# Kernel tuning notes

Measured on AMD Instinct MI355X. Metric: run time of the kernel, lower is better.

## Reference

```python
import jax, jax.numpy as jnp
import numpy as np

B, N, D = 8, 2048, 1024


def setup_inputs() -> dict:
    key = jax.random.key(0)
    k = jax.random.split(key, 6)
    scale = 1.0 / np.sqrt(D)
    x = jax.random.normal(k[0], (B, N, D), dtype=jnp.float32)
    attention_mask = jax.random.randint(k[1], (B, N, N), 0, 2, dtype=jnp.int32)
    W_qkv = jax.random.normal(k[2], (D, 3 * D), dtype=jnp.float32) * scale
    b_qkv = jax.random.normal(k[3], (3 * D,), dtype=jnp.float32) * 0.01
    W_out = jax.random.normal(k[4], (D, D), dtype=jnp.float32) * scale
    b_out = jax.random.normal(k[5], (D,), dtype=jnp.float32) * 0.01
    return {"x": x, "attention_mask": attention_mask, "W_qkv": W_qkv,
            "b_qkv": b_qkv, "W_out": W_out, "b_out": b_out}


def reference(x, attention_mask, W_qkv, b_qkv, W_out, b_out):
    # QKV projection: [B,N,3D]
    qkv = jnp.einsum('bnd,de->bne', x, W_qkv) + b_qkv
    Q, K, V = jnp.split(qkv, 3, axis=-1)
    inv_sqrt_d = jnp.float32(1.0 / np.sqrt(D))
    # naive full [B,N,N] attention scores
    scores = jnp.einsum('bqd,bkd->bqk', Q, K) * inv_sqrt_d
    w = jax.nn.softmax(scores, axis=-1)
    # masked_fill(mask == 0, -1e20) then renormalize (module applies softmax
    # again over the masked weights; dropout is identity in eval mode)
    w = jnp.where(attention_mask == 0, jnp.float32(-1e20), w)
    w = jax.nn.softmax(w, axis=-1)
    out = jnp.einsum('bqk,bkd->bqd', w, V)
    return jnp.einsum('bnd,de->bne', out, W_out) + b_out
```

## Files before the change

kernel.cpp:

```cpp
#include <hip/hip_runtime.h>
#include <hip/hip_bf16.h>

typedef __attribute__((ext_vector_type(8))) short short8;
typedef __attribute__((ext_vector_type(4))) float floatx4;
typedef __attribute__((ext_vector_type(8))) int intx8;

#define AS_GLOBAL(p) ((const __attribute__((address_space(1))) void*)(p))
#define AS_LOCAL(p)  ((__attribute__((address_space(3))) void*)(p))

__device__ __forceinline__ float b2f(unsigned short u) {
    union { unsigned int u; float f; } c; c.u = ((unsigned int)u) << 16; return c.f;
}
__device__ __forceinline__ unsigned short f2b(float f) {
    union { float f; unsigned int u; } c; c.f = f;
    unsigned int u = c.u;
    unsigned int r = (u + 0x7fffu + ((u >> 16) & 1u)) >> 16;
    return (unsigned short)r;
}
__device__ __forceinline__ unsigned char f2fp8(float v) {
    return (unsigned char)(__builtin_amdgcn_cvt_pk_fp8_f32(v, v, 0, false) & 0xff);
}

__global__ __launch_bounds__(256) void cast_x(
    const float* __restrict__ in, unsigned short* __restrict__ xbf,
    unsigned int* __restrict__ xf8, int n4) {
    int i = blockIdx.x * 256 + threadIdx.x;
    if (i >= n4) return;
    float4 v = ((const float4*)in)[i];
    ushort4 o;
    o.x = f2b(v.x); o.y = f2b(v.y); o.z = f2b(v.z); o.w = f2b(v.w);
    ((ushort4*)xbf)[i] = o;
    int p = __builtin_amdgcn_cvt_pk_fp8_f32(v.x, v.y, 0, false);
    p = __builtin_amdgcn_cvt_pk_fp8_f32(v.z, v.w, p, true);
    xf8[i] = (unsigned int)p;
}

__global__ __launch_bounds__(256) void transpose_f32_bf16(
    const float* __restrict__ in, unsigned short* __restrict__ out, int R, int C) {
    __shared__ float t[32][33];
    int c0 = blockIdx.x * 32, r0 = blockIdx.y * 32;
    int tx = threadIdx.x, ty = threadIdx.y;
#pragma unroll
    for (int k = 0; k < 32; k += 8)
        t[ty + k][tx] = in[(size_t)(r0 + ty + k) * C + c0 + tx];
    __syncthreads();
#pragma unroll
    for (int k = 0; k < 32; k += 8)
        out[(size_t)(c0 + ty + k) * R + r0 + tx] = f2b(t[tx][ty + k]);
}

__global__ __launch_bounds__(256) void transpose_f32_fp8_qk(
    const float* __restrict__ in, unsigned char* __restrict__ out) {
    __shared__ float t[32][33];
    int c0 = blockIdx.x * 32, r0 = blockIdx.y * 32;
    int tx = threadIdx.x, ty = threadIdx.y;
#pragma unroll
    for (int k = 0; k < 32; k += 8)
        t[ty + k][tx] = in[(size_t)(r0 + ty + k) * 3072 + c0 + tx];
    __syncthreads();
#pragma unroll
    for (int k = 0; k < 32; k += 8)
        out[(size_t)(c0 + ty + k) * 1024 + r0 + tx] = f2fp8(t[tx][ty + k]);
}

__global__ __launch_bounds__(256) void cast_wv(
    const float* __restrict__ in, unsigned short* __restrict__ out) {
    int i = blockIdx.x * 256 + threadIdx.x;
    int d = i >> 8, rem = (i & 255) * 4;
    float4 v = *(const float4*)&in[(size_t)d * 3072 + 2048 + rem];
    ushort4 o;
    o.x = f2b(v.x); o.y = f2b(v.y); o.z = f2b(v.z); o.w = f2b(v.w);
    *(ushort4*)&out[(size_t)d * 1024 + rem] = o;
}

__global__ __launch_bounds__(256) void bvo_kernel(
    const unsigned short* __restrict__ WoT, const float* __restrict__ bqkv,
    const float* __restrict__ bout, float* __restrict__ bvo) {
    int wv = threadIdx.x >> 6, lane = threadIdx.x & 63;
    int e = blockIdx.x * 4 + wv;
    const unsigned short* row = WoT + (size_t)e * 1024;
    float s = 0.f;
    for (int h = lane; h < 1024; h += 64) s += b2f(row[h]) * bqkv[2048 + h];
#pragma unroll
    for (int o = 32; o; o >>= 1) s += __shfl_xor(s, o);
    if (lane == 0) bvo[e] = s + bout[e];
}

__global__ __launch_bounds__(256) void softmax2_kernel(
    unsigned short* __restrict__ S, const int* __restrict__ mask) {
    const int N = 2048;
    int wv = threadIdx.x >> 6, lane = threadIdx.x & 63;
    size_t row = (size_t)blockIdx.x * 4 + wv;
    unsigned short* srow = S + row * N;
    const int* mrow = mask + row * N;

    float e1[32];
    float l = 0.f;
#pragma unroll
    for (int i = 0; i < 4; ++i) {
        uint4 raw = ((const uint4*)srow)[lane + 64 * i];
        unsigned v[4] = { raw.x, raw.y, raw.z, raw.w };
#pragma unroll
        for (int j = 0; j < 4; ++j) {
            float a = b2f((unsigned short)(v[j] & 0xffff));
            float bb = b2f((unsigned short)(v[j] >> 16));
            float ea = __expf(a), eb = __expf(bb);
            e1[i * 8 + 2 * j] = ea; e1[i * 8 + 2 * j + 1] = eb;
            l += ea + eb;
        }
    }
#pragma unroll
    for (int o = 32; o; o >>= 1) l += __shfl_xor(l, o);
    float invl = 1.0f / l;

    float e2[32];
    float z = 0.f;
#pragma unroll
    for (int i = 0; i < 4; ++i) {
        uint4 m0 = ((const uint4*)mrow)[2 * (lane + 64 * i)];
        uint4 m1 = ((const uint4*)mrow)[2 * (lane + 64 * i) + 1];
        int mk[8] = { (int)m0.x, (int)m0.y, (int)m0.z, (int)m0.w,
                      (int)m1.x, (int)m1.y, (int)m1.z, (int)m1.w };
#pragma unroll
        for (int j = 0; j < 8; ++j) {
            float w1 = e1[i * 8 + j] * invl;
            float e = mk[j] ? __expf(w1) : 0.0f;
            e2[i * 8 + j] = e; z += e;
        }
    }
#pragma unroll
    for (int o = 32; o; o >>= 1) z += __shfl_xor(z, o);
    float invz = (z > 0.f) ? 1.0f / z : 0.0f;
    float fallback = 1.0f / N;
#pragma unroll
    for (int i = 0; i < 4; ++i) {
        float p[8];
#pragma unroll
        for (int j = 0; j < 8; ++j)
            p[j] = (z > 0.f) ? e2[i * 8 + j] * invz : fallback;
        uint4 o;
        o.x = (unsigned)f2b(p[0]) | ((unsigned)f2b(p[1]) << 16);
        o.y = (unsigned)f2b(p[2]) | ((unsigned)f2b(p[3]) << 16);
        o.z = (unsigned)f2b(p[4]) | ((unsigned)f2b(p[5]) << 16);
        o.w = (unsigned)f2b(p[6]) | ((unsigned)f2b(p[7]) << 16);
        ((uint4*)srow)[lane + 64 * i] = o;
    }
}

template <int TAG, bool BIAS, int OUT, int XS, int YS>
__global__ __launch_bounds__(256) void gemm_bt(
    const unsigned short* __restrict__ A, int ldA, long long strideA,
    const unsigned short* __restrict__ B, int ldB, long long strideB,
    void* __restrict__ C, int ldC, long long strideC,
    const float* __restrict__ bias, float scale, int K) {
    __shared__ __align__(16) unsigned short lds[2 * 128 * 64];
    unsigned short* At = lds;
    unsigned short* Bt = lds + 128 * 64;

    unsigned flat = blockIdx.x;
    unsigned wg = (flat & 7u) * (gridDim.x >> 3) + (flat >> 3);
    int bx = wg & ((1u << XS) - 1u);
    int by = (wg >> XS) & ((1u << YS) - 1u);
    int bz = wg >> (XS + YS);

    const unsigned short* Ab = A + (size_t)bz * strideA;
    const unsigned short* Bb = B + (size_t)bz * strideB;
    int tn0 = bx * 128;
    int tm0 = by * 128;
    int tid = threadIdx.x;
    int wave = tid >> 6, lane = tid & 63;
    int lm = lane & 15, q = lane >> 4;
    int wm = (wave >> 1) * 64, wn = (wave & 1) * 64;

    int srow = lane >> 3;
    int sblk = lane & 7;

    floatx4 acc[4][4] = {};

    for (int k0 = 0; k0 < K; k0 += 64) {
        __syncthreads();
#pragma unroll
        for (int i = 0; i < 4; ++i) {
            int chunk = wave * 4 + i;
            int r = chunk * 8 + srow;
            int blk = sblk ^ (r & 7);
            const unsigned short* ga = Ab + (size_t)(tm0 + r) * ldA + (k0 + blk * 8);
            __builtin_amdgcn_global_load_lds(AS_GLOBAL(ga), AS_LOCAL(At + chunk * 512), 16, 0, 0);
            const unsigned short* gb = Bb + (size_t)(tn0 + r) * ldB + (k0 + blk * 8);
            __builtin_amdgcn_global_load_lds(AS_GLOBAL(gb), AS_LOCAL(Bt + chunk * 512), 16, 0, 0);
        }
        __syncthreads();
#pragma unroll
        for (int kk = 0; kk < 2; ++kk) {
            short8 af[4], bf[4];
#pragma unroll
            for (int mt = 0; mt < 4; ++mt) {
                int r = wm + mt * 16 + lm;
                af[mt] = *(const short8*)(At + r * 64 + (((kk * 4 + q) ^ (r & 7)) * 8));
            }
#pragma unroll
            for (int nt = 0; nt < 4; ++nt) {
                int r = wn + nt * 16 + lm;
                bf[nt] = *(const short8*)(Bt + r * 64 + (((kk * 4 + q) ^ (r & 7)) * 8));
            }
#pragma unroll
            for (int mt = 0; mt < 4; ++mt)
#pragma unroll
                for (int nt = 0; nt < 4; ++nt)
                    acc[mt][nt] = __builtin_amdgcn_mfma_f32_16x16x32_bf16(
                        af[mt], bf[nt], acc[mt][nt], 0, 0, 0);
        }
    }

    float biasv[4];
#pragma unroll
    for (int nt = 0; nt < 4; ++nt)
        biasv[nt] = BIAS ? bias[tn0 + wn + nt * 16 + lm] : 0.0f;

    if (OUT == 2) {
        __syncthreads();
        unsigned short* T = lds;
#pragma unroll
        for (int mt = 0; mt < 4; ++mt)
#pragma unroll
            for (int nt = 0; nt < 4; ++nt) {
                int n = wn + nt * 16 + lm;
                int m0 = wm + mt * 16 + q * 4;
                int col = m0 ^ ((n & 15) << 3);
                ushort4 pv;
                float v0 = acc[mt][nt][0] * scale; if (BIAS) v0 += biasv[nt];
                float v1 = acc[mt][nt][1] * scale; if (BIAS) v1 += biasv[nt];
                float v2 = acc[mt][nt][2] * scale; if (BIAS) v2 += biasv[nt];
                float v3 = acc[mt][nt][3] * scale; if (BIAS) v3 += biasv[nt];
                pv.x = f2b(v0); pv.y = f2b(v1); pv.z = f2b(v2); pv.w = f2b(v3);
                *(ushort4*)&T[n * 128 + col] = pv;
            }
        __syncthreads();
        unsigned short* Cb = (unsigned short*)C + (size_t)(tm0 >> 11) * strideC + (tm0 & 2047);
#pragma unroll
        for (int r8 = 0; r8 < 8; ++r8) {
            int idx = tid + 256 * r8;
            int d = idx >> 4, c = idx & 15;
            int cs = (c ^ (d & 15)) << 3;
            short8 v = *(const short8*)&T[d * 128 + cs];
            *(short8*)&Cb[(size_t)(tn0 + d) * ldC + c * 8] = v;
        }
        return;
    }

#pragma unroll
    for (int mt = 0; mt < 4; ++mt) {
#pragma unroll
        for (int nt = 0; nt < 4; ++nt) {
            int gm = tm0 + wm + mt * 16 + q * 4;
            int gn = tn0 + wn + nt * 16 + lm;
#pragma unroll
            for (int r = 0; r < 4; ++r) {
                float v = acc[mt][nt][r] * scale;
                if (BIAS) v += biasv[nt];
                size_t idx = (size_t)bz * strideC + (size_t)(gm + r) * ldC + gn;
                if (OUT == 1) ((float*)C)[idx] = v;
                else          ((unsigned short*)C)[idx] = f2b(v);
            }
        }
    }
}

template <int TAG, bool BIAS, bool OUTFP8, int XS, int YS>
__global__ __launch_bounds__(256) void gemm_f8_bt(
    const unsigned char* __restrict__ A, int ldA, long long strideA,
    const unsigned char* __restrict__ B, int ldB, long long strideB,
    void* __restrict__ C, int ldC, long long strideC,
    const float* __restrict__ bias, float scale, int K) {
    __shared__ __align__(16) unsigned char lds[2 * 128 * 128];
    unsigned char* At = lds;
    unsigned char* Bt = lds + 128 * 128;

    unsigned flat = blockIdx.x;
    unsigned wg = (flat & 7u) * (gridDim.x >> 3) + (flat >> 3);
    int bx = wg & ((1u << XS) - 1u);
    int by = (wg >> XS) & ((1u << YS) - 1u);
    int bz = wg >> (XS + YS);

    const unsigned char* Ab = A + (size_t)bz * strideA;
    const unsigned char* Bb = B + (size_t)bz * strideB;
    int tn0 = bx * 128;
    int tm0 = by * 128;
    int tid = threadIdx.x;
    int wave = tid >> 6, lane = tid & 63;
    int lm = lane & 15, q = lane >> 4;
    int q2 = q * 2;
    int wm = (wave >> 1) * 64, wn = (wave & 1) * 64;

    int srow = lane >> 3;
    int sblk = lane & 7;

    floatx4 acc[4][4] = {};

    for (int k0 = 0; k0 < K; k0 += 128) {
        __syncthreads();
#pragma unroll
        for (int i = 0; i < 4; ++i) {
            int chunk = wave * 4 + i;
            int r = chunk * 8 + srow;
            int blk = sblk ^ (r & 7);
            const unsigned char* ga = Ab + (size_t)(tm0 + r) * ldA + (k0 + blk * 16);
            __builtin_amdgcn_global_load_lds(AS_GLOBAL(ga), AS_LOCAL(At + chunk * 1024), 16, 0, 0);
            const unsigned char* gb = Bb + (size_t)(tn0 + r) * ldB + (k0 + blk * 16);
            __builtin_amdgcn_global_load_lds(AS_GLOBAL(gb), AS_LOCAL(Bt + chunk * 1024), 16, 0, 0);
        }
        __syncthreads();
        intx8 af[4], bf[4];
#pragma unroll
        for (int mt = 0; mt < 4; ++mt) {
            int r = wm + mt * 16 + lm;
            const unsigned char* base = At + r * 128;
            int4 lo = *(const int4*)(base + ((q2 ^ (r & 7)) << 4));
            int4 hi = *(const int4*)(base + (((q2 + 1) ^ (r & 7)) << 4));
            af[mt][0] = lo.x; af[mt][1] = lo.y; af[mt][2] = lo.z; af[mt][3] = lo.w;
            af[mt][4] = hi.x; af[mt][5] = hi.y; af[mt][6] = hi.z; af[mt][7] = hi.w;
        }
#pragma unroll
        for (int nt = 0; nt < 4; ++nt) {
            int r = wn + nt * 16 + lm;
            const unsigned char* base = Bt + r * 128;
            int4 lo = *(const int4*)(base + ((q2 ^ (r & 7)) << 4));
            int4 hi = *(const int4*)(base + (((q2 + 1) ^ (r & 7)) << 4));
            bf[nt][0] = lo.x; bf[nt][1] = lo.y; bf[nt][2] = lo.z; bf[nt][3] = lo.w;
            bf[nt][4] = hi.x; bf[nt][5] = hi.y; bf[nt][6] = hi.z; bf[nt][7] = hi.w;
        }
#pragma unroll
        for (int mt = 0; mt < 4; ++mt)
#pragma unroll
            for (int nt = 0; nt < 4; ++nt)
                acc[mt][nt] = __builtin_amdgcn_mfma_scale_f32_16x16x128_f8f6f4(
                    af[mt], bf[nt], acc[mt][nt], 0, 0,
                    0, 0x7f7f7f7f, 0, 0x7f7f7f7f);
    }

    float biasv[4];
#pragma unroll
    for (int nt = 0; nt < 4; ++nt)
        biasv[nt] = BIAS ? bias[tn0 + wn + nt * 16 + lm] : 0.0f;
#pragma unroll
    for (int mt = 0; mt < 4; ++mt) {
#pragma unroll
        for (int nt = 0; nt < 4; ++nt) {
            int gm = tm0 + wm + mt * 16 + q * 4;
            int gn = tn0 + wn + nt * 16 + lm;
#pragma unroll
            for (int r = 0; r < 4; ++r) {
                float v = acc[mt][nt][r] * scale;
                if (BIAS) v += biasv[nt];
                size_t idx = (size_t)bz * strideC + (size_t)(gm + r) * ldC + gn;
                if (OUTFP8) ((unsigned char*)C)[idx] = f2fp8(v);
                else        ((unsigned short*)C)[idx] = f2b(v);
            }
        }
    }
}

extern "C" void kernel_launch(void* const* d_in, const int* in_sizes, int n_in,
                              void* d_out, int out_size, void* d_ws, size_t ws_size,
                              hipStream_t stream) {
    const float* x    = (const float*)d_in[0];
    const int*   mask = (const int*)d_in[1];
    const float* Wqkv = (const float*)d_in[2];
    const float* bqkv = (const float*)d_in[3];
    const float* Wout = (const float*)d_in[4];
    const float* bout = (const float*)d_in[5];
    float* out = (float*)d_out;

    char* w = (char*)d_ws;
    unsigned short* x_bf  = (unsigned short*)(w);
    unsigned char*  x_f8  = (unsigned char*)(w + 33554432);
    unsigned char*  QKf8  = (unsigned char*)(w + 50331648);
    unsigned short* VpT   = (unsigned short*)(w + 117440512);
    unsigned short* S     = (unsigned short*)(w + 150994944);
    unsigned char*  WqkT8 = (unsigned char*)(w + 218103808);
    unsigned short* WoT   = (unsigned short*)(w + 220200960);
    unsigned short* Wv_bf = (unsigned short*)(w + 222298112);
    unsigned short* WvoT  = (unsigned short*)(w + 224395264);
    float*          bvo   = (float*)(w + 226492416);

    cast_x<<<16384, 256, 0, stream>>>(x, x_bf, (unsigned int*)x_f8, 4194304);
    transpose_f32_fp8_qk<<<dim3(64, 32), dim3(32, 8), 0, stream>>>(Wqkv, WqkT8);
    transpose_f32_bf16<<<dim3(32, 32), dim3(32, 8), 0, stream>>>(Wout, WoT, 1024, 1024);
    cast_wv<<<1024, 256, 0, stream>>>(Wqkv, Wv_bf);
    bvo_kernel<<<256, 256, 0, stream>>>(WoT, bqkv, bout, bvo);

    gemm_bt<4, false, 0, 3, 3><<<64, 256, 0, stream>>>(
        WoT, 1024, 0, Wv_bf, 1024, 0, WvoT, 1024, 0, nullptr, 1.0f, 1024);

    gemm_f8_bt<0, true, true, 4, 7><<<2048, 256, 0, stream>>>(
        x_f8, 1024, 0, WqkT8, 1024, 0, QKf8, 2048, 0, bqkv, 1.0f, 1024);

    gemm_bt<5, true, 2, 3, 7><<<1024, 256, 0, stream>>>(
        x_bf, 1024, 0, WvoT, 1024, 0, VpT, 2048, 1024LL * 2048, bvo, 1.0f, 1024);

    gemm_f8_bt<1, false, false, 4, 4><<<2048, 256, 0, stream>>>(
        QKf8, 2048, 2048LL * 2048, QKf8 + 1024, 2048, 2048LL * 2048,
        S, 2048, 2048LL * 2048, nullptr, 0.03125f, 1024);

    softmax2_kernel<<<4096, 256, 0, stream>>>(S, mask);

    gemm_bt<2, false, 1, 3, 4><<<1024, 256, 0, stream>>>(
        S, 2048, 2048LL * 2048, VpT, 2048, 1024LL * 2048,
        out, 1024, 2048LL * 1024, nullptr, 1.0f, 2048);
}
```

Before: 530.2 us.

## Add 256x256-tile 8-wave bf16 GEMM with double-buffered LDS for PV product

Replaces the final attention-times-V GEMM (previously 128x128 tiles, 256 threads) with a new kernel using 256x256 output tiles, 8 waves, and double-buffered LDS filled through direct global-to-LDS loads with an XOR swizzle. Loads for the next K-tile are interleaved with four MFMA phases separated by barriers and priority bumps. The goal is higher arithmetic intensity and better overlap of memory with MFMA. In exchange it uses 128KB of LDS and a large accumulator register footprint, and the grid shrinks to 256 blocks, which may underfill the CUs.

```diff
diff --git a/kernel.cpp b/kernel.cpp
--- a/kernel.cpp
+++ b/kernel.cpp
@@ -266,6 +266,160 @@
     }
 }
 
+template <int MH>
+__device__ __forceinline__ void mfma16(floatx4 (&acc)[8][4], const short8 (&af)[4],
+                                       const short8 (&bf)[4]) {
+#pragma unroll
+    for (int m = 0; m < 4; ++m)
+#pragma unroll
+        for (int n = 0; n < 4; ++n)
+            acc[MH * 4 + m][n] = __builtin_amdgcn_mfma_f32_16x16x32_bf16(
+                af[m], bf[n], acc[MH * 4 + m][n], 0, 0, 0);
+}
+
+template <int NXB, int NYB>
+__global__ __launch_bounds__(512, 2) void gemm_bt8(
+    const unsigned short* __restrict__ A, int ldA, long long strideA,
+    const unsigned short* __restrict__ B, int ldB, long long strideB,
+    float* __restrict__ C, int ldC, long long strideC,
+    float scale, int K) {
+    __shared__ __align__(16) unsigned short lds[65536];
+    constexpr int TILE = 16384;
+    constexpr int BREG = 32768;
+
+    int tid = threadIdx.x;
+    int wave = tid >> 6, lane = tid & 63;
+    int lm = lane & 15, q = lane >> 4;
+    int wmi = wave >> 2, wni = wave & 3;
+
+    unsigned flat = blockIdx.x;
+    unsigned wg = (flat & 7u) * (gridDim.x >> 3) + (flat >> 3);
+    int bx = wg % NXB;
+    int rem = wg / NXB;
+    int by = rem % NYB;
+    int bz = rem / NYB;
+    int tn0 = bx * 256, tm0 = by * 256;
+
+    const unsigned short* Ab = A + (size_t)bz * strideA;
+    const unsigned short* Bb = B + (size_t)bz * strideB;
+
+    int srow8 = lane >> 3, s7 = lane & 7;
+    const unsigned short* gA[4];
+    const unsigned short* gB[4];
+#pragma unroll
+    for (int i = 0; i < 4; ++i) {
+        int r = i * 64 + wave * 8 + srow8;
+        int blk = s7 ^ (r & 7);
+        gA[i] = Ab + (size_t)(tm0 + r) * ldA + blk * 8;
+        gB[i] = Bb + (size_t)(tn0 + r) * ldB + blk * 8;
+    }
+
+    int nt = K >> 6;
+
+#pragma unroll
+    for (int i = 0; i < 4; ++i)
+        __builtin_amdgcn_global_load_lds(AS_GLOBAL(gB[i]), AS_LOCAL(lds + BREG + i * 4096 + wave * 512), 16, 0, 0);
+#pragma unroll
+    for (int i = 0; i < 4; ++i)
+        __builtin_amdgcn_global_load_lds(AS_GLOBAL(gA[i]), AS_LOCAL(lds + i * 4096 + wave * 512), 16, 0, 0);
+#pragma unroll
+    for (int i = 0; i < 4; ++i) { gA[i] += 64; gB[i] += 64; }
+
+    asm volatile("s_waitcnt vmcnt(0)" ::: "memory");
+    __builtin_amdgcn_s_barrier();
+
+    floatx4 acc[8][4] = {};
+    short8 bf0[4], bf1[4];
+    short8 af[4];
+
+    int aOff = (wmi * 128 + lm) * 64;
+    int bOff = (wni * 64 + lm) * 64;
+    int sl0 = (q ^ (lm & 7)) * 8;
+    int sl1 = ((4 + q) ^ (lm & 7)) * 8;
+
+    for (int t = 0; t < nt; ++t) {
+        unsigned short* Ap = lds + (t & 1) * TILE;
+        unsigned short* Bp = lds + BREG + (t & 1) * TILE;
+        unsigned short* An = lds + ((t + 1) & 1) * TILE;
+        unsigned short* Bn = lds + BREG + ((t + 1) & 1) * TILE;
+        bool pre = (t + 1) < nt;
+
+#pragma unroll
+        for (int n = 0; n < 4; ++n) bf0[n] = *(const short8*)(Bp + bOff + n * 1024 + sl0);
+#pragma unroll
+        for (int n = 0; n < 4; ++n) bf1[n] = *(const short8*)(Bp + bOff + n * 1024 + sl1);
+#pragma unroll
+        for (int m = 0; m < 4; ++m) af[m] = *(const short8*)(Ap + aOff + m * 1024 + sl0);
+        if (pre) {
+#pragma unroll
+            for (int i = 0; i < 4; ++i)
+                __builtin_amdgcn_global_load_lds(AS_GLOBAL(gB[i]), AS_LOCAL(Bn + i * 4096 + wave * 512), 16, 0, 0);
+        }
+        __builtin_amdgcn_sched_barrier(0);
+        __builtin_amdgcn_s_barrier();
+        asm volatile("s_waitcnt lgkmcnt(0)" ::: "memory");
+        __builtin_amdgcn_sched_barrier(0);
+        __builtin_amdgcn_s_setprio(1);
+        mfma16<0>(acc, af, bf0);
+        __builtin_amdgcn_s_setprio(0);
+        __builtin_amdgcn_s_barrier();
+
+#pragma unroll
+        for (int m = 0; m < 4; ++m) af[m] = *(const short8*)(Ap + aOff + 4096 + m * 1024 + sl0);
+        if (pre) {
+#pragma unroll
+            for (int i = 0; i < 4; ++i)
+                __builtin_amdgcn_global_load_lds(AS_GLOBAL(gA[i]), AS_LOCAL(An + i * 4096 + wave * 512), 16, 0, 0);
+#pragma unroll
+            for (int i = 0; i < 4; ++i) { gA[i] += 64; gB[i] += 64; }
+        }
+        __builtin_amdgcn_sched_barrier(0);
+        __builtin_amdgcn_s_barrier();
+        asm volatile("s_waitcnt lgkmcnt(0)" ::: "memory");
+        __builtin_amdgcn_sched_barrier(0);
+        __builtin_amdgcn_s_setprio(1);
+        mfma16<1>(acc, af, bf0);
+        __builtin_amdgcn_s_setprio(0);
+        __builtin_amdgcn_s_barrier();
+
+#pragma unroll
+        for (int m = 0; m < 4; ++m) af[m] = *(const short8*)(Ap + aOff + m * 1024 + sl1);
+        __builtin_amdgcn_sched_barrier(0);
+        __builtin_amdgcn_s_barrier();
+        asm volatile("s_waitcnt lgkmcnt(0)" ::: "memory");
+        __builtin_amdgcn_sched_barrier(0);
+        __builtin_amdgcn_s_setprio(1);
+        mfma16<0>(acc, af, bf1);
+        __builtin_amdgcn_s_setprio(0);
+        __builtin_amdgcn_s_barrier();
+
+#pragma unroll
+        for (int m = 0; m < 4; ++m) af[m] = *(const short8*)(Ap + aOff + 4096 + m * 1024 + sl1);
+        __builtin_amdgcn_sched_barrier(0);
+        __builtin_amdgcn_s_barrier();
+        asm volatile("s_waitcnt lgkmcnt(0)" ::: "memory");
+        __builtin_amdgcn_sched_barrier(0);
+        __builtin_amdgcn_s_setprio(1);
+        mfma16<1>(acc, af, bf1);
+        __builtin_amdgcn_s_setprio(0);
+        asm volatile("s_waitcnt vmcnt(0)" ::: "memory");
+        __builtin_amdgcn_s_barrier();
+    }
+
+    float* Cb = C + (size_t)bz * strideC;
+#pragma unroll
+    for (int m = 0; m < 8; ++m) {
+#pragma unroll
+        for (int n = 0; n < 4; ++n) {
+            int gm = tm0 + wmi * 128 + m * 16 + q * 4;
+            int gn = tn0 + wni * 64 + n * 16 + lm;
+#pragma unroll
+            for (int r = 0; r < 4; ++r)
+                Cb[(size_t)(gm + r) * ldC + gn] = acc[m][n][r] * scale;
+        }
+    }
+}
+
 template <int TAG, bool BIAS, bool OUTFP8, int XS, int YS>
 __global__ __launch_bounds__(256) void gemm_f8_bt(
     const unsigned char* __restrict__ A, int ldA, long long strideA,
@@ -404,7 +558,7 @@
 
     softmax2_kernel<<<4096, 256, 0, stream>>>(S, mask);
 
-    gemm_bt<2, false, 1, 3, 4><<<1024, 256, 0, stream>>>(
+    gemm_bt8<4, 8><<<256, 512, 0, stream>>>(
         S, 2048, 2048LL * 2048, VpT, 2048, 1024LL * 2048,
-        out, 1024, 2048LL * 1024, nullptr, 1.0f, 2048);
-}
+        out, 1024, 2048LL * 1024, 1.0f, 2048);
+}
```

Result: faster. 500.3 us (-5.7%).
